# Kernel tuning notes

Measured on AMD Instinct MI355X. Metric: run time of the kernel, lower is better.

Reference implementation:

```python
import jax, jax.numpy as jnp
import numpy as np

N, E, D, H, G = 50000, 800000, 128, 128, 64
EPS = 1e-5


def setup_inputs() -> dict:
    key = jax.random.key(0)
    ks = jax.random.split(key, 16)
    x = jax.random.normal(ks[0], (N, D), dtype=jnp.float32)
    edge_index = jax.random.randint(ks[1], (2, E), 0, N, dtype=jnp.int64)
    batch = jnp.sort(jax.random.randint(ks[2], (N,), 0, G, dtype=jnp.int64))
    dims = [D, H, H, H]
    params = {}
    for i in range(3):
        params[f"W{i}"] = jax.random.normal(ks[3 + i], (dims[i], dims[i + 1]), dtype=jnp.float32) * (1.0 / np.sqrt(dims[i]).astype(np.float32))
        params[f"b{i}"] = jnp.zeros((dims[i + 1],), jnp.float32)
        params[f"g{i}"] = jnp.ones((dims[i + 1],), jnp.float32)   # BN gamma
        params[f"be{i}"] = jnp.zeros((dims[i + 1],), jnp.float32)  # BN beta
    params["Wout"] = jax.random.normal(ks[10], (H, 1), dtype=jnp.float32) * (1.0 / np.sqrt(H).astype(np.float32))
    params["bout"] = jnp.zeros((1,), jnp.float32)
    return {"x": x, "edge_index": edge_index, "batch": batch, **params}


def _gcn_forward(x, edge_index, batch, Ws, bs, gs, bes, Wout, bout):
    n = x.shape[0]
    loop = jnp.arange(n)
    # GCNConv default: add self-loops, symmetric degree normalization
    src = jnp.concatenate([edge_index[0], loop])
    dst = jnp.concatenate([edge_index[1], loop])
    deg = jax.ops.segment_sum(jnp.ones_like(dst, x.dtype), dst, num_segments=n)
    dinv = jax.lax.rsqrt(jnp.maximum(deg, 1.0))  # deg >= 1 from self-loops
    norm = dinv[src] * dinv[dst]                 # [E+N]
    h = x
    for W, b, g, be in zip(Ws, bs, gs, bes):
        h = h @ W                                               # transform [N,C]
        msg = h[src] * norm[:, None]                            # gather [E+N,C]
        h = jax.ops.segment_sum(msg, dst, num_segments=n) + b   # scatter-add
        # BatchNorm1d (training-mode batch statistics over nodes)
        mu = jnp.mean(h, axis=0)
        var = jnp.var(h, axis=0)
        h = (h - mu) * jax.lax.rsqrt(var + EPS) * g + be
        h = jax.nn.relu(h)
        # dropout: identity (deterministic eval reference)
    counts = jax.ops.segment_sum(jnp.ones((n,), h.dtype), batch, num_segments=G)
    pooled = jax.ops.segment_sum(h, batch, num_segments=G) / jnp.maximum(counts, 1.0)[:, None]
    return jax.nn.sigmoid(pooled @ Wout + bout)  # [G,1]


def reference(x, edge_index, batch, W0, b0, g0, be0, W1, b1, g1, be1, W2, b2, g2, be2, Wout, bout):
    return _gcn_forward(x, edge_index, batch,
                        (W0, W1, W2), (b0, b1, b2), (g0, g1, g2), (be0, be1, be2),
                        Wout, bout)
```

## Files before the change

### kernel.cpp

```cpp
#include <hip/hip_runtime.h>

#define EPSBN 1e-5f
#define AGG_BLOCKS 2048

using bf16x8 = __attribute__((ext_vector_type(8))) short;
using f32x4  = __attribute__((ext_vector_type(4))) float;

__device__ __forceinline__ unsigned short f2bf(float f) {
    unsigned u = __builtin_bit_cast(unsigned, f);
    unsigned r = (u + 0x7FFFu + ((u >> 16) & 1u)) >> 16;
    return (unsigned short)r;
}
__device__ __forceinline__ float bf2f(unsigned short s) {
    unsigned u = ((unsigned)s) << 16;
    return __builtin_bit_cast(float, u);
}


__global__ __launch_bounds__(256) void k_bhist(const int* __restrict__ dst, int E,
                                               int* __restrict__ deg, int* __restrict__ bcnt, int shift) {
    __shared__ int lh[512];
    for (int i = threadIdx.x; i < 512; i += 256) lh[i] = 0;
    __syncthreads();
    for (int i = blockIdx.x * blockDim.x + threadIdx.x; i < E; i += gridDim.x * blockDim.x) {
        int d = dst[i];
        atomicAdd(&deg[d], 1);
        atomicAdd(&lh[d >> shift], 1);
    }
    __syncthreads();
    for (int i = threadIdx.x; i < 512; i += 256)
        if (lh[i]) atomicAdd(&bcnt[i], lh[i]);
}

__global__ void k_dinv(const int* __restrict__ deg, int N, float* __restrict__ dinv) {
    int i = blockIdx.x * blockDim.x + threadIdx.x;
    if (i < N) dinv[i] = rsqrtf((float)(deg[i] + 1));
}

__global__ void k_scan1(const int* __restrict__ deg, int N, int* __restrict__ rs, int* __restrict__ blk) {
    __shared__ int sh[256];
    int tid = threadIdx.x;
    int i = blockIdx.x * 256 + tid;
    int v = (i < N) ? deg[i] : 0;
    sh[tid] = v; __syncthreads();
    for (int off = 1; off < 256; off <<= 1) {
        int t = (tid >= off) ? sh[tid - off] : 0;
        __syncthreads();
        sh[tid] += t;
        __syncthreads();
    }
    if (i < N) rs[i] = sh[tid] - v;
    if (tid == 255) blk[blockIdx.x] = sh[255];
}

__global__ void k_scan2(const int* __restrict__ blk, int nb, int* __restrict__ blkoff) {
    __shared__ int sh[1024];
    int tid = threadIdx.x;
    int v = (tid < nb) ? blk[tid] : 0;
    sh[tid] = v; __syncthreads();
    for (int off = 1; off < 1024; off <<= 1) {
        int t = (tid >= off) ? sh[tid - off] : 0;
        __syncthreads();
        sh[tid] += t;
        __syncthreads();
    }
    if (tid < nb) blkoff[tid] = sh[tid] - v;
}

__global__ void k_scan3(int* __restrict__ rs, int N, const int* __restrict__ blkoff) {
    int i = blockIdx.x * blockDim.x + threadIdx.x;
    if (i < N) rs[i] += blkoff[i >> 8];
}


__global__ __launch_bounds__(256) void k_bscatter(const int* __restrict__ src, const int* __restrict__ dst, int E,
                                                  const int* __restrict__ boff, int* __restrict__ gcur,
                                                  uint2* __restrict__ ebuf, int shift) {
    __shared__ int lh[512], lb[512];
    int tid = threadIdx.x;
    int base = blockIdx.x * 2048;
    for (int i = tid; i < 512; i += 256) lh[i] = 0;
    __syncthreads();
    int ms[8], md[8];
    #pragma unroll
    for (int j = 0; j < 8; ++j) {
        int idx = base + j * 256 + tid;
        if (idx < E) {
            ms[j] = src[idx]; md[j] = dst[idx];
            atomicAdd(&lh[md[j] >> shift], 1);
        } else md[j] = -1;
    }
    __syncthreads();
    for (int b = tid; b < 512; b += 256) {
        int c = lh[b];
        lb[b] = c ? atomicAdd(&gcur[b], c) : 0;
    }
    __syncthreads();
    for (int i = tid; i < 512; i += 256) lh[i] = 0;
    __syncthreads();
    #pragma unroll
    for (int j = 0; j < 8; ++j) {
        if (md[j] >= 0) {
            int b = md[j] >> shift;
            int r = atomicAdd(&lh[b], 1);
            ebuf[boff[b] + lb[b] + r] = make_uint2((unsigned)ms[j], (unsigned)md[j]);
        }
    }
}


__global__ __launch_bounds__(256) void k_fill2(const uint2* __restrict__ ebuf, const int* __restrict__ bcnt,
                                               const int* __restrict__ boff, const int* __restrict__ rs,
                                               const float* __restrict__ dinv,
                                               uint2* __restrict__ colw, int shift) {
    __shared__ int lcur[256];
    int b = blockIdx.x;
    int n0 = b << shift;
    int cnt = bcnt[b], s = boff[b];
    int span = 1 << shift;
    for (int i = threadIdx.x; i < span; i += 256) lcur[i] = 0;
    __syncthreads();
    for (int i = threadIdx.x; i < cnt; i += 256) {
        uint2 e = ebuf[s + i];
        int d = (int)e.y;
        int sv = (int)e.x;
        int pos = rs[d] + atomicAdd(&lcur[d - n0], 1);
        colw[pos] = make_uint2((unsigned)sv, __builtin_bit_cast(unsigned, dinv[sv]));
    }
}


__global__ __launch_bounds__(256) void k_wprep(const float* __restrict__ W0, const float* __restrict__ W1,
                                               const float* __restrict__ W2, unsigned short* __restrict__ Wimg) {
    const float* W = (blockIdx.x == 0) ? W0 : (blockIdx.x == 1) ? W1 : W2;
    unsigned short* out = Wimg + (size_t)blockIdx.x * 16384;
    int tid = threadIdx.x;
    int n = tid & 127, kh = tid >> 7;
    const float* wp = &W[(kh * 64) * 128 + n];
    #pragma unroll
    for (int kb = 0; kb < 8; ++kb) {
        unsigned short t8[8];
        #pragma unroll
        for (int e = 0; e < 8; ++e)
            t8[e] = f2bf(wp[(kb * 8 + e) * 128]);
        int byte = (n * 256 + kh * 128 + kb * 16) ^ ((n & 7) << 4);
        *reinterpret_cast<uint4*>(reinterpret_cast<char*>(out) + byte) =
            *reinterpret_cast<const uint4*>(t8);
    }
}


__global__ __launch_bounds__(256) void k_gemm(const unsigned short* __restrict__ Abf,
                                              const float* __restrict__ Af,
                                              const unsigned short* __restrict__ Wimg,
                                              unsigned short* __restrict__ C, int N,
                                              const float* __restrict__ scale,
                                              const float* __restrict__ shift, int mode) {
    __shared__ unsigned short Asw[128 * 128];
    __shared__ unsigned short Wt[128 * 128];
    int tid = threadIdx.x;
    int r0 = blockIdx.x * 128;

    {
        const uint4* wi = reinterpret_cast<const uint4*>(Wimg);
        uint4* wl = reinterpret_cast<uint4*>(Wt);
        #pragma unroll
        for (int j = 0; j < 8; ++j)
            wl[tid + j * 256] = wi[tid + j * 256];
    }
    if (mode == 0) {
        const float* ap = &Af[(size_t)r0 * 128];
        #pragma unroll
        for (int j = 0; j < 8; ++j) {
            int u = tid + j * 256;
            int row = u >> 4, cg = u & 15;
            unsigned short t8[8] = {0,0,0,0,0,0,0,0};
            if (r0 + row < N) {
                float4 a0 = *reinterpret_cast<const float4*>(ap + row * 128 + cg * 8);
                float4 a1 = *reinterpret_cast<const float4*>(ap + row * 128 + cg * 8 + 4);
                t8[0]=f2bf(a0.x); t8[1]=f2bf(a0.y); t8[2]=f2bf(a0.z); t8[3]=f2bf(a0.w);
                t8[4]=f2bf(a1.x); t8[5]=f2bf(a1.y); t8[6]=f2bf(a1.z); t8[7]=f2bf(a1.w);
            }
            int byte = (row * 256 + cg * 16) ^ ((row & 7) << 4);
            *reinterpret_cast<uint4*>(reinterpret_cast<char*>(Asw) + byte) =
                *reinterpret_cast<const uint4*>(t8);
        }
    } else {
        const unsigned short* ap = &Abf[(size_t)r0 * 128];
        #pragma unroll
        for (int j = 0; j < 8; ++j) {
            int u = tid + j * 256;
            int row = u >> 4, cg = u & 15;
            unsigned short t8[8] = {0,0,0,0,0,0,0,0};
            if (r0 + row < N) {
                ushort4 v0 = *reinterpret_cast<const ushort4*>(ap + (size_t)row * 128 + cg * 8);
                ushort4 v1 = *reinterpret_cast<const ushort4*>(ap + (size_t)row * 128 + cg * 8 + 4);
                float4 sc0 = *reinterpret_cast<const float4*>(&scale[cg * 8]);
                float4 sc1 = *reinterpret_cast<const float4*>(&scale[cg * 8 + 4]);
                float4 sf0 = *reinterpret_cast<const float4*>(&shift[cg * 8]);
                float4 sf1 = *reinterpret_cast<const float4*>(&shift[cg * 8 + 4]);
                t8[0] = f2bf(fmaxf(bf2f(v0.x) * sc0.x + sf0.x, 0.f));
                t8[1] = f2bf(fmaxf(bf2f(v0.y) * sc0.y + sf0.y, 0.f));
                t8[2] = f2bf(fmaxf(bf2f(v0.z) * sc0.z + sf0.z, 0.f));
                t8[3] = f2bf(fmaxf(bf2f(v0.w) * sc0.w + sf0.w, 0.f));
                t8[4] = f2bf(fmaxf(bf2f(v1.x) * sc1.x + sf1.x, 0.f));
                t8[5] = f2bf(fmaxf(bf2f(v1.y) * sc1.y + sf1.y, 0.f));
                t8[6] = f2bf(fmaxf(bf2f(v1.z) * sc1.z + sf1.z, 0.f));
                t8[7] = f2bf(fmaxf(bf2f(v1.w) * sc1.w + sf1.w, 0.f));
            }
            int byte = (row * 256 + cg * 16) ^ ((row & 7) << 4);
            *reinterpret_cast<uint4*>(reinterpret_cast<char*>(Asw) + byte) =
                *reinterpret_cast<const uint4*>(t8);
        }
    }
    __syncthreads();

    int wv = tid >> 6, lane = tid & 63;
    int lr = lane & 15, lk = lane >> 4;
    f32x4 acc[2][8] = {};
    #pragma unroll
    for (int kk = 0; kk < 4; ++kk) {
        bf16x8 af[2], bf[8];
        #pragma unroll
        for (int mf = 0; mf < 2; ++mf) {
            int ar = wv * 32 + mf * 16 + lr;
            int byte = (ar * 256 + kk * 64 + lk * 16) ^ ((ar & 7) << 4);
            af[mf] = *reinterpret_cast<const bf16x8*>(reinterpret_cast<const char*>(Asw) + byte);
        }
        #pragma unroll
        for (int nf = 0; nf < 8; ++nf) {
            int bn = nf * 16 + lr;
            int byte = (bn * 256 + kk * 64 + lk * 16) ^ ((bn & 7) << 4);
            bf[nf] = *reinterpret_cast<const bf16x8*>(reinterpret_cast<const char*>(Wt) + byte);
        }
        #pragma unroll
        for (int mf = 0; mf < 2; ++mf)
            #pragma unroll
            for (int nf = 0; nf < 8; ++nf)
                acc[mf][nf] = __builtin_amdgcn_mfma_f32_16x16x32_bf16(af[mf], bf[nf], acc[mf][nf], 0, 0, 0);
    }
    __syncthreads();
    #pragma unroll
    for (int mf = 0; mf < 2; ++mf)
        #pragma unroll
        for (int nf = 0; nf < 8; ++nf)
            #pragma unroll
            for (int r = 0; r < 4; ++r) {
                int row = wv * 32 + mf * 16 + lk * 4 + r;
                int colc = nf * 16 + lr;
                Asw[row * 128 + colc] = f2bf(acc[mf][nf][r]);
            }
    __syncthreads();
    #pragma unroll
    for (int j = 0; j < 8; ++j) {
        int u = tid + j * 256;
        int row = u >> 4, cg = u & 15;
        if (r0 + row < N)
            *reinterpret_cast<uint4*>(&C[((size_t)(r0 + row)) * 128 + cg * 8]) =
                *reinterpret_cast<const uint4*>(&Asw[row * 128 + cg * 8]);
    }
}


__global__ __launch_bounds__(256) void k_agg(const unsigned short* __restrict__ t, const uint2* __restrict__ colw,
                                             const int* __restrict__ rs, const int* __restrict__ deg,
                                             const float* __restrict__ dinv, const float* __restrict__ bias,
                                             unsigned short* __restrict__ out, int N,
                                             float* __restrict__ p1, float* __restrict__ p2) {
    __shared__ uint2 ec[4][64];
    __shared__ float sh[4][64][4];
    int wv = threadIdx.x >> 6, lane = threadIdx.x & 63;
    const ushort2* tp = reinterpret_cast<const ushort2*>(t);
    float b0 = bias[2 * lane], b1 = bias[2 * lane + 1];
    float s1x = 0.f, s1y = 0.f, s2x = 0.f, s2y = 0.f;
    for (int w = blockIdx.x * 4 + wv; w < N; w += gridDim.x * 4) {
        int start = rs[w], cnt = deg[w];
        float di = dinv[w];
        float ax = 0.f, ay = 0.f;
        for (int base = 0; base < cnt; base += 64) {
            int m = min(cnt - base, 64);
            if (lane < m) ec[wv][lane] = colw[start + base + lane];
            asm volatile("s_waitcnt lgkmcnt(0)" ::: "memory");
            int e = 0;
            for (; e + 4 <= m; e += 4) {
                uint2 e0 = ec[wv][e], e1 = ec[wv][e + 1], e2 = ec[wv][e + 2], e3 = ec[wv][e + 3];
                ushort2 v0 = tp[(size_t)e0.x * 64 + lane];
                ushort2 v1 = tp[(size_t)e1.x * 64 + lane];
                ushort2 v2 = tp[(size_t)e2.x * 64 + lane];
                ushort2 v3 = tp[(size_t)e3.x * 64 + lane];
                float w0 = __builtin_bit_cast(float, e0.y), w1 = __builtin_bit_cast(float, e1.y);
                float w2 = __builtin_bit_cast(float, e2.y), w3 = __builtin_bit_cast(float, e3.y);
                ax += w0 * bf2f(v0.x) + w1 * bf2f(v1.x) + w2 * bf2f(v2.x) + w3 * bf2f(v3.x);
                ay += w0 * bf2f(v0.y) + w1 * bf2f(v1.y) + w2 * bf2f(v2.y) + w3 * bf2f(v3.y);
            }
            for (; e < m; ++e) {
                uint2 ee = ec[wv][e];
                ushort2 v = tp[(size_t)ee.x * 64 + lane];
                float ww = __builtin_bit_cast(float, ee.y);
                ax += ww * bf2f(v.x);
                ay += ww * bf2f(v.y);
            }
        }
        ushort2 self = tp[(size_t)w * 64 + lane];
        ushort2 o;
        o.x = f2bf(di * ax + di * di * bf2f(self.x) + b0);
        o.y = f2bf(di * ay + di * di * bf2f(self.y) + b1);
        reinterpret_cast<ushort2*>(out)[(size_t)w * 64 + lane] = o;
        float rx = bf2f(o.x), ry = bf2f(o.y);
        s1x += rx; s1y += ry; s2x += rx * rx; s2y += ry * ry;
    }
    sh[wv][lane][0] = s1x; sh[wv][lane][1] = s1y; sh[wv][lane][2] = s2x; sh[wv][lane][3] = s2y;
    __syncthreads();
    int tid = threadIdx.x;
    if (tid < 64) {
        float a0 = 0.f, a1 = 0.f, a2 = 0.f, a3 = 0.f;
        #pragma unroll
        for (int r = 0; r < 4; ++r) {
            a0 += sh[r][tid][0]; a1 += sh[r][tid][1];
            a2 += sh[r][tid][2]; a3 += sh[r][tid][3];
        }
        p1[blockIdx.x * 128 + 2 * tid]     = a0;
        p1[blockIdx.x * 128 + 2 * tid + 1] = a1;
        p2[blockIdx.x * 128 + 2 * tid]     = a2;
        p2[blockIdx.x * 128 + 2 * tid + 1] = a3;
    }
}


__global__ __launch_bounds__(128) void k_statsmid(const float* __restrict__ p1, const float* __restrict__ p2,
                                                  int rows, float* __restrict__ pm1, float* __restrict__ pm2) {
    int c = threadIdx.x, b = blockIdx.x;
    int r0 = b * rows;
    float s1 = 0.f, s2 = 0.f;
    #pragma unroll 4
    for (int r = 0; r < rows; ++r) {
        s1 += p1[(size_t)(r0 + r) * 128 + c];
        s2 += p2[(size_t)(r0 + r) * 128 + c];
    }
    pm1[b * 128 + c] = s1;
    pm2[b * 128 + c] = s2;
}

__global__ __launch_bounds__(1024) void k_stats2(const float* __restrict__ p1, const float* __restrict__ p2,
                                                 int nb, int N,
                                                 const float* __restrict__ g, const float* __restrict__ be,
                                                 float* __restrict__ scale, float* __restrict__ shift) {
    __shared__ double sh1[1024], sh2[1024];
    int tid = threadIdx.x;
    int c = tid & 127, seg = tid >> 7;
    double s1 = 0.0, s2 = 0.0;
    int b = seg;
    for (; b + 32 <= nb; b += 32) {
        double a0 = p1[(b      ) * 128 + c], q0 = p2[(b      ) * 128 + c];
        double a1 = p1[(b +  8) * 128 + c], q1 = p2[(b +  8) * 128 + c];
        double a2 = p1[(b + 16) * 128 + c], q2 = p2[(b + 16) * 128 + c];
        double a3 = p1[(b + 24) * 128 + c], q3 = p2[(b + 24) * 128 + c];
        s1 += (a0 + a1) + (a2 + a3);
        s2 += (q0 + q1) + (q2 + q3);
    }
    for (; b < nb; b += 8) { s1 += p1[b * 128 + c]; s2 += p2[b * 128 + c]; }
    sh1[tid] = s1; sh2[tid] = s2;
    __syncthreads();
    #pragma unroll
    for (int s = 4; s >= 1; s >>= 1) {
        if (seg < s) {
            sh1[tid] += sh1[tid + s * 128];
            sh2[tid] += sh2[tid + s * 128];
        }
        __syncthreads();
    }
    if (tid < 128) {
        double mu = sh1[c] / N;
        double var = sh2[c] / N - mu * mu;
        double inv = 1.0 / sqrt(var + (double)EPSBN);
        scale[c] = (float)((double)g[c] * inv);
        shift[c] = (float)((double)be[c] - mu * (double)g[c] * inv);
    }
// ... 57 lines not shown
__global__ void k_final(const float* __restrict__ pool, const int* __restrict__ cnt,
                        const float* __restrict__ bout, int G, float* __restrict__ out) {
    int g = blockIdx.x * blockDim.x + threadIdx.x;
    if (g < G) {
        float c = fmaxf((float)cnt[g], 1.f);
        float p = pool[g] / c + bout[0];
        out[g] = 1.f / (1.f + expf(-p));
    }
}


extern "C" void kernel_launch(void* const* d_in, const int* in_sizes, int n_in,
                              void* d_out, int out_size, void* d_ws, size_t ws_size,
                              hipStream_t stream) {
    const float* x    = (const float*)d_in[0];
    const int*   ei   = (const int*)d_in[1];
    const int*   batch= (const int*)d_in[2];
    const float* W0p  = (const float*)d_in[3];
    const float* b0p  = (const float*)d_in[4];
    const float* g0p  = (const float*)d_in[5];
    const float* be0p = (const float*)d_in[6];
    const float* W1p  = (const float*)d_in[7];
    const float* b1p  = (const float*)d_in[8];
    const float* g1p  = (const float*)d_in[9];
    const float* be1p = (const float*)d_in[10];
    const float* W2p  = (const float*)d_in[11];
    const float* b2p  = (const float*)d_in[12];
    const float* g2p  = (const float*)d_in[13];
    const float* be2p = (const float*)d_in[14];
    const float* Woutp= (const float*)d_in[15];
    const float* boutp= (const float*)d_in[16];

    int N = in_sizes[0] / 128;
    int E = in_sizes[1] / 2;
    int G = out_size;
    const int* src = ei;
    const int* dst = ei + E;

    int shiftB = 7;
    while ((((N + (1 << shiftB) - 1) >> shiftB) > 512) && shiftB < 8) ++shiftB;
    int nbuck = (N + (1 << shiftB) - 1) >> shiftB;

    char* p = (char*)d_ws;
    auto alloc = [&](size_t bytes) {
        void* q = (void*)p;
        p += (bytes + 255) & ~(size_t)255;
        return q;
    };
    unsigned short* Bt  = (unsigned short*)alloc((size_t)N * 128 * 2);
    unsigned short* Bh  = (unsigned short*)alloc((size_t)N * 128 * 2);
    uint2*  colw   = (uint2*) alloc((size_t)E * 8);
    uint2*  ebuf   = (uint2*) alloc((size_t)E * 8);
    int*    rsA    = (int*)   alloc((size_t)N * 4);
    int*    deg    = (int*)   alloc((size_t)N * 4);
    float*  dinv   = (float*) alloc((size_t)N * 4);
    int*    blk    = (int*)   alloc(1024 * 4);
    int*    blkoff = (int*)   alloc(1024 * 4);
    int*    bcnt   = (int*)   alloc(512 * 4);
    int*    boff   = (int*)   alloc(512 * 4);
    int*    gcur   = (int*)   alloc(512 * 4);
    unsigned short* Wimg = (unsigned short*)alloc(3 * 16384 * 2);
    float*  p1     = (float*) alloc((size_t)AGG_BLOCKS * 128 * 4);
    float*  p2     = (float*) alloc((size_t)AGG_BLOCKS * 128 * 4);
    float*  pm1    = (float*) alloc(128 * 128 * 4);
    float*  pm2    = (float*) alloc(128 * 128 * 4);
    float*  scale  = (float*) alloc(128 * 4);
    float*  shift  = (float*) alloc(128 * 4);
    float*  pool   = (float*) alloc(64 * 4);
    int*    cnt    = (int*)   alloc(64 * 4);

    hipMemsetAsync(deg, 0, (size_t)N * 4, stream);
    hipMemsetAsync(bcnt, 0, 512 * 4, stream);
    hipMemsetAsync(gcur, 0, 512 * 4, stream);
    hipMemsetAsync(pool, 0, 64 * 4, stream);
    hipMemsetAsync(cnt, 0, 64 * 4, stream);

    int nb = (N + 255) / 256;
    k_wprep   <<<3, 256, 0, stream>>>(W0p, W1p, W2p, Wimg);
    k_bhist   <<<256, 256, 0, stream>>>(dst, E, deg, bcnt, shiftB);
    k_dinv    <<<nb, 256, 0, stream>>>(deg, N, dinv);
    k_scan1   <<<nb, 256, 0, stream>>>(deg, N, rsA, blk);
    k_scan2   <<<1, 1024, 0, stream>>>(blk, nb, blkoff);
    k_scan3   <<<nb, 256, 0, stream>>>(rsA, N, blkoff);
    k_scan2   <<<1, 1024, 0, stream>>>(bcnt, 512, boff);
    k_bscatter<<<(E + 2047) / 2048, 256, 0, stream>>>(src, dst, E, boff, gcur, ebuf, shiftB);
    k_fill2   <<<nbuck, 256, 0, stream>>>(ebuf, bcnt, boff, rsA, dinv, colw, shiftB);

    int gemmBlocks = (N + 127) / 128;
    int midRows = AGG_BLOCKS / 128;

    k_gemm    <<<gemmBlocks, 256, 0, stream>>>(nullptr, x, Wimg, Bt, N, scale, shift, 0);
    k_agg     <<<AGG_BLOCKS, 256, 0, stream>>>(Bt, colw, rsA, deg, dinv, b0p, Bh, N, p1, p2);
    k_statsmid<<<128, 128, 0, stream>>>(p1, p2, midRows, pm1, pm2);
    k_stats2  <<<1, 1024, 0, stream>>>(pm1, pm2, 128, N, g0p, be0p, scale, shift);
    k_gemm    <<<gemmBlocks, 256, 0, stream>>>(Bh, nullptr, Wimg + 16384, Bt, N, scale, shift, 1);
    k_agg     <<<AGG_BLOCKS, 256, 0, stream>>>(Bt, colw, rsA, deg, dinv, b1p, Bh, N, p1, p2);
    k_statsmid<<<128, 128, 0, stream>>>(p1, p2, midRows, pm1, pm2);
    k_stats2  <<<1, 1024, 0, stream>>>(pm1, pm2, 128, N, g1p, be1p, scale, shift);
    k_gemm    <<<gemmBlocks, 256, 0, stream>>>(Bh, nullptr, Wimg + 32768, Bt, N, scale, shift, 1);
    k_agg     <<<AGG_BLOCKS, 256, 0, stream>>>(Bt, colw, rsA, deg, dinv, b2p, Bh, N, p1, p2);
    k_statsmid<<<128, 128, 0, stream>>>(p1, p2, midRows, pm1, pm2);
    k_stats2  <<<1, 1024, 0, stream>>>(pm1, pm2, 128, N, g2p, be2p, scale, shift);
    k_pool <<<256, 256, 0, stream>>>(Bh, batch, scale, shift, Woutp, N, G, pool, cnt);
    k_final<<<1, 64, 0, stream>>>(pool, cnt, boutp, G, (float*)d_out);
}
```

Measured before the change: 290.4 us.

## Vectorize aggregation gathers, shrink GEMM tile, fuse dinv into scan, merge memsets

The aggregation kernel now has each quarter-wave gather a full 128-column row as 16-byte loads, so one wave processes four edges at once. Partial sums are combined with cross-lane shuffles before the output and BatchNorm statistics are written. The GEMM row tile drops from 128 to 64 rows to launch more blocks. The dinv computation moves into the first scan kernel, and the five memsets collapse into one contiguous memset. Together these cut per-edge load instruction count and launch overhead, but the aggregation kernel adds shuffle work and higher register pressure from the 8-wide accumulators.

```diff
diff --git a/kernel.cpp b/kernel.cpp
--- a/kernel.cpp
+++ b/kernel.cpp
@@ -16,6 +16,17 @@
     return __builtin_bit_cast(float, u);
 }
 
+__device__ __forceinline__ void acc8(float* ax, uint4 r, float w) {
+    unsigned rr[4] = {r.x, r.y, r.z, r.w};
+    #pragma unroll
+    for (int j = 0; j < 4; ++j) {
+        float lo = __builtin_bit_cast(float, rr[j] << 16);
+        float hi = __builtin_bit_cast(float, rr[j] & 0xFFFF0000u);
+        ax[2 * j]     += w * lo;
+        ax[2 * j + 1] += w * hi;
+    }
+}
+
 
 __global__ __launch_bounds__(256) void k_bhist(const int* __restrict__ dst, int E,
                                                int* __restrict__ deg, int* __restrict__ bcnt, int shift) {
@@ -32,16 +43,13 @@
         if (lh[i]) atomicAdd(&bcnt[i], lh[i]);
 }
 
-__global__ void k_dinv(const int* __restrict__ deg, int N, float* __restrict__ dinv) {
-    int i = blockIdx.x * blockDim.x + threadIdx.x;
-    if (i < N) dinv[i] = rsqrtf((float)(deg[i] + 1));
-}
-
-__global__ void k_scan1(const int* __restrict__ deg, int N, int* __restrict__ rs, int* __restrict__ blk) {
+__global__ void k_scan1(const int* __restrict__ deg, int N, int* __restrict__ rs, int* __restrict__ blk,
+                        float* __restrict__ dinv) {
     __shared__ int sh[256];
     int tid = threadIdx.x;
     int i = blockIdx.x * 256 + tid;
     int v = (i < N) ? deg[i] : 0;
+    if (i < N) dinv[i] = rsqrtf((float)(v + 1));
     sh[tid] = v; __syncthreads();
     for (int off = 1; off < 256; off <<= 1) {
         int t = (tid >= off) ? sh[tid - off] : 0;
@@ -156,10 +164,10 @@
                                               unsigned short* __restrict__ C, int N,
                                               const float* __restrict__ scale,
                                               const float* __restrict__ shift, int mode) {
-    __shared__ unsigned short Asw[128 * 128];
+    __shared__ unsigned short Asw[64 * 128];
     __shared__ unsigned short Wt[128 * 128];
     int tid = threadIdx.x;
-    int r0 = blockIdx.x * 128;
+    int r0 = blockIdx.x * 64;
 
     {
         const uint4* wi = reinterpret_cast<const uint4*>(Wimg);
@@ -171,7 +179,7 @@
     if (mode == 0) {
         const float* ap = &Af[(size_t)r0 * 128];
         #pragma unroll
-        for (int j = 0; j < 8; ++j) {
+        for (int j = 0; j < 4; ++j) {
             int u = tid + j * 256;
             int row = u >> 4, cg = u & 15;
             unsigned short t8[8] = {0,0,0,0,0,0,0,0};
@@ -188,7 +196,7 @@
     } else {
         const unsigned short* ap = &Abf[(size_t)r0 * 128];
         #pragma unroll
-        for (int j = 0; j < 8; ++j) {
+        for (int j = 0; j < 4; ++j) {
             int u = tid + j * 256;
             int row = u >> 4, cg = u & 15;
             unsigned short t8[8] = {0,0,0,0,0,0,0,0};
@@ -217,16 +225,13 @@
 
     int wv = tid >> 6, lane = tid & 63;
     int lr = lane & 15, lk = lane >> 4;
-    f32x4 acc[2][8] = {};
+    f32x4 acc[8] = {};
     #pragma unroll
     for (int kk = 0; kk < 4; ++kk) {
-        bf16x8 af[2], bf[8];
-        #pragma unroll
-        for (int mf = 0; mf < 2; ++mf) {
-            int ar = wv * 32 + mf * 16 + lr;
-            int byte = (ar * 256 + kk * 64 + lk * 16) ^ ((ar & 7) << 4);
-            af[mf] = *reinterpret_cast<const bf16x8*>(reinterpret_cast<const char*>(Asw) + byte);
-        }
+        int ar = wv * 16 + lr;
+        int abyte = (ar * 256 + kk * 64 + lk * 16) ^ ((ar & 7) << 4);
+        bf16x8 af = *reinterpret_cast<const bf16x8*>(reinterpret_cast<const char*>(Asw) + abyte);
+        bf16x8 bf[8];
         #pragma unroll
         for (int nf = 0; nf < 8; ++nf) {
             int bn = nf * 16 + lr;
@@ -234,25 +239,21 @@
             bf[nf] = *reinterpret_cast<const bf16x8*>(reinterpret_cast<const char*>(Wt) + byte);
         }
         #pragma unroll
-        for (int mf = 0; mf < 2; ++mf)
-            #pragma unroll
-            for (int nf = 0; nf < 8; ++nf)
-                acc[mf][nf] = __builtin_amdgcn_mfma_f32_16x16x32_bf16(af[mf], bf[nf], acc[mf][nf], 0, 0, 0);
-    }
-    __syncthreads();
-    #pragma unroll
-    for (int mf = 0; mf < 2; ++mf)
-        #pragma unroll
         for (int nf = 0; nf < 8; ++nf)
-            #pragma unroll
-            for (int r = 0; r < 4; ++r) {
-                int row = wv * 32 + mf * 16 + lk * 4 + r;
-                int colc = nf * 16 + lr;
-                Asw[row * 128 + colc] = f2bf(acc[mf][nf][r]);
-            }
-    __syncthreads();
-    #pragma unroll
-    for (int j = 0; j < 8; ++j) {
+            acc[nf] = __builtin_amdgcn_mfma_f32_16x16x32_bf16(af, bf[nf], acc[nf], 0, 0, 0);
+    }
+    __syncthreads();
+    #pragma unroll
+    for (int nf = 0; nf < 8; ++nf)
+        #pragma unroll
+        for (int r = 0; r < 4; ++r) {
+            int row = wv * 16 + lk * 4 + r;
+            int colc = nf * 16 + lr;
+            Asw[row * 128 + colc] = f2bf(acc[nf][r]);
+        }
+    __syncthreads();
+    #pragma unroll
+    for (int j = 0; j < 4; ++j) {
         int u = tid + j * 256;
         int row = u >> 4, cg = u & 15;
         if (r0 + row < N)
@@ -268,61 +269,87 @@
                                              unsigned short* __restrict__ out, int N,
                                              float* __restrict__ p1, float* __restrict__ p2) {
     __shared__ uint2 ec[4][64];
-    __shared__ float sh[4][64][4];
+    __shared__ float shs[4][16][8][2];
     int wv = threadIdx.x >> 6, lane = threadIdx.x & 63;
-    const ushort2* tp = reinterpret_cast<const ushort2*>(t);
-    float b0 = bias[2 * lane], b1 = bias[2 * lane + 1];
-    float s1x = 0.f, s1y = 0.f, s2x = 0.f, s2y = 0.f;
+    int q = lane >> 4, l = lane & 15;
+    const uint4* tp8 = reinterpret_cast<const uint4*>(t);
+    float b8[8];
+    {
+        float4 ba = *reinterpret_cast<const float4*>(&bias[l * 8]);
+        float4 bb = *reinterpret_cast<const float4*>(&bias[l * 8 + 4]);
+        b8[0]=ba.x; b8[1]=ba.y; b8[2]=ba.z; b8[3]=ba.w;
+        b8[4]=bb.x; b8[5]=bb.y; b8[6]=bb.z; b8[7]=bb.w;
+    }
+    float s1[8] = {}, s2[8] = {};
     for (int w = blockIdx.x * 4 + wv; w < N; w += gridDim.x * 4) {
         int start = rs[w], cnt = deg[w];
         float di = dinv[w];
-        float ax = 0.f, ay = 0.f;
+        float ax[8] = {};
         for (int base = 0; base < cnt; base += 64) {
             int m = min(cnt - base, 64);
             if (lane < m) ec[wv][lane] = colw[start + base + lane];
             asm volatile("s_waitcnt lgkmcnt(0)" ::: "memory");
-            int e = 0;
-            for (; e + 4 <= m; e += 4) {
-                uint2 e0 = ec[wv][e], e1 = ec[wv][e + 1], e2 = ec[wv][e + 2], e3 = ec[wv][e + 3];
-                ushort2 v0 = tp[(size_t)e0.x * 64 + lane];
-                ushort2 v1 = tp[(size_t)e1.x * 64 + lane];
-                ushort2 v2 = tp[(size_t)e2.x * 64 + lane];
-                ushort2 v3 = tp[(size_t)e3.x * 64 + lane];
-                float w0 = __builtin_bit_cast(float, e0.y), w1 = __builtin_bit_cast(float, e1.y);
-                float w2 = __builtin_bit_cast(float, e2.y), w3 = __builtin_bit_cast(float, e3.y);
-                ax += w0 * bf2f(v0.x) + w1 * bf2f(v1.x) + w2 * bf2f(v2.x) + w3 * bf2f(v3.x);
-                ay += w0 * bf2f(v0.y) + w1 * bf2f(v1.y) + w2 * bf2f(v2.y) + w3 * bf2f(v3.y);
+            int steps = m >> 2, rem = m & 3;
+            int s = 0;
+            for (; s + 2 <= steps; s += 2) {
+                uint2 m0 = ec[wv][(s << 2) + q];
+                uint2 m1 = ec[wv][(s << 2) + 4 + q];
+                uint4 r0 = tp8[(size_t)m0.x * 16 + l];
+                uint4 r1 = tp8[(size_t)m1.x * 16 + l];
+                acc8(ax, r0, __builtin_bit_cast(float, m0.y));
+                acc8(ax, r1, __builtin_bit_cast(float, m1.y));
             }
-            for (; e < m; ++e) {
-                uint2 ee = ec[wv][e];
-                ushort2 v = tp[(size_t)ee.x * 64 + lane];
-                float ww = __builtin_bit_cast(float, ee.y);
-                ax += ww * bf2f(v.x);
-                ay += ww * bf2f(v.y);
+            if (s < steps) {
+                uint2 m0 = ec[wv][(s << 2) + q];
+                uint4 r0 = tp8[(size_t)m0.x * 16 + l];
+                acc8(ax, r0, __builtin_bit_cast(float, m0.y));
             }
-        }
-        ushort2 self = tp[(size_t)w * 64 + lane];
-        ushort2 o;
-        o.x = f2bf(di * ax + di * di * bf2f(self.x) + b0);
-        o.y = f2bf(di * ay + di * di * bf2f(self.y) + b1);
-        reinterpret_cast<ushort2*>(out)[(size_t)w * 64 + lane] = o;
-        float rx = bf2f(o.x), ry = bf2f(o.y);
-        s1x += rx; s1y += ry; s2x += rx * rx; s2y += ry * ry;
-    }
-    sh[wv][lane][0] = s1x; sh[wv][lane][1] = s1y; sh[wv][lane][2] = s2x; sh[wv][lane][3] = s2y;
-    __syncthreads();
-    int tid = threadIdx.x;
-    if (tid < 64) {
-        float a0 = 0.f, a1 = 0.f, a2 = 0.f, a3 = 0.f;
-        #pragma unroll
-        for (int r = 0; r < 4; ++r) {
-            a0 += sh[r][tid][0]; a1 += sh[r][tid][1];
-            a2 += sh[r][tid][2]; a3 += sh[r][tid][3];
-        }
-        p1[blockIdx.x * 128 + 2 * tid]     = a0;
-        p1[blockIdx.x * 128 + 2 * tid + 1] = a1;
-        p2[blockIdx.x * 128 + 2 * tid]     = a2;
-        p2[blockIdx.x * 128 + 2 * tid + 1] = a3;
+            if (q < rem) {
+                uint2 m0 = ec[wv][(steps << 2) + q];
+                uint4 r0 = tp8[(size_t)m0.x * 16 + l];
+                acc8(ax, r0, __builtin_bit_cast(float, m0.y));
+            }
+        }
+        #pragma unroll
+        for (int j = 0; j < 8; ++j) {
+            float v = ax[j];
+            v += __shfl_down(v, 32);
+            v += __shfl_down(v, 16);
+            ax[j] = v;
+        }
+        if (q == 0) {
+            uint4 sr = tp8[(size_t)w * 16 + l];
+            unsigned sw_[4] = {sr.x, sr.y, sr.z, sr.w};
+            unsigned short ov[8];
+            float d2 = di * di;
+            #pragma unroll
+            for (int j = 0; j < 8; ++j) {
+                unsigned uw = sw_[j >> 1];
+                float sv = (j & 1) ? __builtin_bit_cast(float, uw & 0xFFFF0000u)
+                                   : __builtin_bit_cast(float, uw << 16);
+                float r = di * ax[j] + d2 * sv + b8[j];
+                unsigned short us = f2bf(r);
+                ov[j] = us;
+                float rr = bf2f(us);
+                s1[j] += rr; s2[j] += rr * rr;
+            }
+            *reinterpret_cast<uint4*>(&out[(size_t)w * 128 + l * 8]) =
+                *reinterpret_cast<const uint4*>(ov);
+        }
+    }
+    if (q == 0) {
+        #pragma unroll
+        for (int j = 0; j < 8; ++j) { shs[wv][l][j][0] = s1[j]; shs[wv][l][j][1] = s2[j]; }
+    }
+    __syncthreads();
+    int tid = threadIdx.x;
+    if (tid < 128) {
+        int ll = tid >> 3, jj = tid & 7;
+        float a1 = 0.f, a2 = 0.f;
+        #pragma unroll
+        for (int r = 0; r < 4; ++r) { a1 += shs[r][ll][jj][0]; a2 += shs[r][ll][jj][1]; }
+        p1[blockIdx.x * 128 + tid] = a1;
+        p2[blockIdx.x * 128 + tid] = a2;
     }
 }
 
@@ -486,13 +513,10 @@
     uint2*  colw   = (uint2*) alloc((size_t)E * 8);
     uint2*  ebuf   = (uint2*) alloc((size_t)E * 8);
     int*    rsA    = (int*)   alloc((size_t)N * 4);
-    int*    deg    = (int*)   alloc((size_t)N * 4);
     float*  dinv   = (float*) alloc((size_t)N * 4);
     int*    blk    = (int*)   alloc(1024 * 4);
     int*    blkoff = (int*)   alloc(1024 * 4);
-    int*    bcnt   = (int*)   alloc(512 * 4);
     int*    boff   = (int*)   alloc(512 * 4);
-    int*    gcur   = (int*)   alloc(512 * 4);
     unsigned short* Wimg = (unsigned short*)alloc(3 * 16384 * 2);
     float*  p1     = (float*) alloc((size_t)AGG_BLOCKS * 128 * 4);
     float*  p2     = (float*) alloc((size_t)AGG_BLOCKS * 128 * 4);
@@ -500,27 +524,27 @@
     float*  pm2    = (float*) alloc(128 * 128 * 4);
     float*  scale  = (float*) alloc(128 * 4);
     float*  shift  = (float*) alloc(128 * 4);
+    char*   z0     = p;
+    int*    deg    = (int*)   alloc((size_t)N * 4);
+    int*    bcnt   = (int*)   alloc(512 * 4);
+    int*    gcur   = (int*)   alloc(512 * 4);
     float*  pool   = (float*) alloc(64 * 4);
     int*    cnt    = (int*)   alloc(64 * 4);
-
-    hipMemsetAsync(deg, 0, (size_t)N * 4, stream);
-    hipMemsetAsync(bcnt, 0, 512 * 4, stream);
-    hipMemsetAsync(gcur, 0, 512 * 4, stream);
-    hipMemsetAsync(pool, 0, 64 * 4, stream);
-    hipMemsetAsync(cnt, 0, 64 * 4, stream);
+    size_t  zbytes = (size_t)(p - z0);
+
+    hipMemsetAsync(z0, 0, zbytes, stream);
 
     int nb = (N + 255) / 256;
     k_wprep   <<<3, 256, 0, stream>>>(W0p, W1p, W2p, Wimg);
     k_bhist   <<<256, 256, 0, stream>>>(dst, E, deg, bcnt, shiftB);
-    k_dinv    <<<nb, 256, 0, stream>>>(deg, N, dinv);
-    k_scan1   <<<nb, 256, 0, stream>>>(deg, N, rsA, blk);
+    k_scan1   <<<nb, 256, 0, stream>>>(deg, N, rsA, blk, dinv);
     k_scan2   <<<1, 1024, 0, stream>>>(blk, nb, blkoff);
     k_scan3   <<<nb, 256, 0, stream>>>(rsA, N, blkoff);
     k_scan2   <<<1, 1024, 0, stream>>>(bcnt, 512, boff);
     k_bscatter<<<(E + 2047) / 2048, 256, 0, stream>>>(src, dst, E, boff, gcur, ebuf, shiftB);
     k_fill2   <<<nbuck, 256, 0, stream>>>(ebuf, bcnt, boff, rsA, dinv, colw, shiftB);
 
-    int gemmBlocks = (N + 127) / 128;
+    int gemmBlocks = (N + 63) / 64;
     int midRows = AGG_BLOCKS / 128;
 
     k_gemm    <<<gemmBlocks, 256, 0, stream>>>(nullptr, x, Wimg, Bt, N, scale, shift, 0);
```

Result: slower. 315.4 us (+8.6%).

## Fuse dinv into scan, halve GEMM tile, dual-node aggregation, merge memsets

Applied to the files above, without the earlier changes.

Computes dinv inside the first scan kernel, which removes one launch. The GEMM row tile shrinks from 128 to 64 rows per block, giving more blocks and less shared memory per block. The aggregation kernel now processes two destination nodes per wavefront at once to raise memory-level parallelism on the gathers. The zero-initialised buffers are placed next to each other and cleared with one memset instead of five. Interleaving two nodes risks imbalance when the two degrees differ, and the smaller tile reloads W more often.

```diff
diff --git a/kernel.cpp b/kernel.cpp
--- a/kernel.cpp
+++ b/kernel.cpp
@@ -32,16 +32,13 @@
         if (lh[i]) atomicAdd(&bcnt[i], lh[i]);
 }
 
-__global__ void k_dinv(const int* __restrict__ deg, int N, float* __restrict__ dinv) {
-    int i = blockIdx.x * blockDim.x + threadIdx.x;
-    if (i < N) dinv[i] = rsqrtf((float)(deg[i] + 1));
-}
-
-__global__ void k_scan1(const int* __restrict__ deg, int N, int* __restrict__ rs, int* __restrict__ blk) {
+__global__ void k_scan1(const int* __restrict__ deg, int N, int* __restrict__ rs, int* __restrict__ blk,
+                        float* __restrict__ dinv) {
     __shared__ int sh[256];
     int tid = threadIdx.x;
     int i = blockIdx.x * 256 + tid;
     int v = (i < N) ? deg[i] : 0;
+    if (i < N) dinv[i] = rsqrtf((float)(v + 1));
     sh[tid] = v; __syncthreads();
     for (int off = 1; off < 256; off <<= 1) {
         int t = (tid >= off) ? sh[tid - off] : 0;
@@ -156,10 +153,10 @@
                                               unsigned short* __restrict__ C, int N,
                                               const float* __restrict__ scale,
                                               const float* __restrict__ shift, int mode) {
-    __shared__ unsigned short Asw[128 * 128];
+    __shared__ unsigned short Asw[64 * 128];
     __shared__ unsigned short Wt[128 * 128];
     int tid = threadIdx.x;
-    int r0 = blockIdx.x * 128;
+    int r0 = blockIdx.x * 64;
 
     {
         const uint4* wi = reinterpret_cast<const uint4*>(Wimg);
@@ -171,7 +168,7 @@
     if (mode == 0) {
         const float* ap = &Af[(size_t)r0 * 128];
         #pragma unroll
-        for (int j = 0; j < 8; ++j) {
+        for (int j = 0; j < 4; ++j) {
             int u = tid + j * 256;
             int row = u >> 4, cg = u & 15;
             unsigned short t8[8] = {0,0,0,0,0,0,0,0};
@@ -188,7 +185,7 @@
     } else {
         const unsigned short* ap = &Abf[(size_t)r0 * 128];
         #pragma unroll
-        for (int j = 0; j < 8; ++j) {
+        for (int j = 0; j < 4; ++j) {
             int u = tid + j * 256;
             int row = u >> 4, cg = u & 15;
             unsigned short t8[8] = {0,0,0,0,0,0,0,0};
@@ -217,16 +214,13 @@
 
     int wv = tid >> 6, lane = tid & 63;
     int lr = lane & 15, lk = lane >> 4;
-    f32x4 acc[2][8] = {};
+    f32x4 acc[8] = {};
     #pragma unroll
     for (int kk = 0; kk < 4; ++kk) {
-        bf16x8 af[2], bf[8];
-        #pragma unroll
-        for (int mf = 0; mf < 2; ++mf) {
-            int ar = wv * 32 + mf * 16 + lr;
-            int byte = (ar * 256 + kk * 64 + lk * 16) ^ ((ar & 7) << 4);
-            af[mf] = *reinterpret_cast<const bf16x8*>(reinterpret_cast<const char*>(Asw) + byte);
-        }
+        int ar = wv * 16 + lr;
+        int abyte = (ar * 256 + kk * 64 + lk * 16) ^ ((ar & 7) << 4);
+        bf16x8 af = *reinterpret_cast<const bf16x8*>(reinterpret_cast<const char*>(Asw) + abyte);
+        bf16x8 bf[8];
         #pragma unroll
         for (int nf = 0; nf < 8; ++nf) {
             int bn = nf * 16 + lr;
@@ -234,25 +228,21 @@
             bf[nf] = *reinterpret_cast<const bf16x8*>(reinterpret_cast<const char*>(Wt) + byte);
         }
         #pragma unroll
-        for (int mf = 0; mf < 2; ++mf)
-            #pragma unroll
-            for (int nf = 0; nf < 8; ++nf)
-                acc[mf][nf] = __builtin_amdgcn_mfma_f32_16x16x32_bf16(af[mf], bf[nf], acc[mf][nf], 0, 0, 0);
-    }
-    __syncthreads();
-    #pragma unroll
-    for (int mf = 0; mf < 2; ++mf)
-        #pragma unroll
         for (int nf = 0; nf < 8; ++nf)
-            #pragma unroll
-            for (int r = 0; r < 4; ++r) {
-                int row = wv * 32 + mf * 16 + lk * 4 + r;
-                int colc = nf * 16 + lr;
-                Asw[row * 128 + colc] = f2bf(acc[mf][nf][r]);
-            }
-    __syncthreads();
-    #pragma unroll
-    for (int j = 0; j < 8; ++j) {
+            acc[nf] = __builtin_amdgcn_mfma_f32_16x16x32_bf16(af, bf[nf], acc[nf], 0, 0, 0);
+    }
+    __syncthreads();
+    #pragma unroll
+    for (int nf = 0; nf < 8; ++nf)
+        #pragma unroll
+        for (int r = 0; r < 4; ++r) {
+            int row = wv * 16 + lk * 4 + r;
+            int colc = nf * 16 + lr;
+            Asw[row * 128 + colc] = f2bf(acc[nf][r]);
+        }
+    __syncthreads();
+    #pragma unroll
+    for (int j = 0; j < 4; ++j) {
         int u = tid + j * 256;
         int row = u >> 4, cg = u & 15;
         if (r0 + row < N)
@@ -267,47 +257,82 @@
                                              const float* __restrict__ dinv, const float* __restrict__ bias,
                                              unsigned short* __restrict__ out, int N,
                                              float* __restrict__ p1, float* __restrict__ p2) {
-    __shared__ uint2 ec[4][64];
+    __shared__ uint2 ec[4][2][64];
     __shared__ float sh[4][64][4];
     int wv = threadIdx.x >> 6, lane = threadIdx.x & 63;
     const ushort2* tp = reinterpret_cast<const ushort2*>(t);
     float b0 = bias[2 * lane], b1 = bias[2 * lane + 1];
     float s1x = 0.f, s1y = 0.f, s2x = 0.f, s2y = 0.f;
-    for (int w = blockIdx.x * 4 + wv; w < N; w += gridDim.x * 4) {
-        int start = rs[w], cnt = deg[w];
-        float di = dinv[w];
-        float ax = 0.f, ay = 0.f;
-        for (int base = 0; base < cnt; base += 64) {
-            int m = min(cnt - base, 64);
-            if (lane < m) ec[wv][lane] = colw[start + base + lane];
+    int stride = gridDim.x * 4;
+    for (int w = blockIdx.x * 4 + wv; w < N; w += 2 * stride) {
+        int wB = w + stride;
+        bool hasB = wB < N;
+        int stA = rs[w], cntA = deg[w];
+        int stB = hasB ? rs[wB] : 0, cntB = hasB ? deg[wB] : 0;
+        float diA = dinv[w], diB = hasB ? dinv[wB] : 0.f;
+        float axA = 0.f, ayA = 0.f, axB = 0.f, ayB = 0.f;
+        int maxc = max(cntA, cntB);
+        for (int base = 0; base < maxc; base += 64) {
+            int mA = min(cntA - base, 64);
+            int mB = min(cntB - base, 64);
+            if (lane < mA) ec[wv][0][lane] = colw[stA + base + lane];
+            if (lane < mB) ec[wv][1][lane] = colw[stB + base + lane];
             asm volatile("s_waitcnt lgkmcnt(0)" ::: "memory");
+            int both = min(mA, mB);
             int e = 0;
-            for (; e + 4 <= m; e += 4) {
-                uint2 e0 = ec[wv][e], e1 = ec[wv][e + 1], e2 = ec[wv][e + 2], e3 = ec[wv][e + 3];
-                ushort2 v0 = tp[(size_t)e0.x * 64 + lane];
-                ushort2 v1 = tp[(size_t)e1.x * 64 + lane];
-                ushort2 v2 = tp[(size_t)e2.x * 64 + lane];
-                ushort2 v3 = tp[(size_t)e3.x * 64 + lane];
-                float w0 = __builtin_bit_cast(float, e0.y), w1 = __builtin_bit_cast(float, e1.y);
-                float w2 = __builtin_bit_cast(float, e2.y), w3 = __builtin_bit_cast(float, e3.y);
-                ax += w0 * bf2f(v0.x) + w1 * bf2f(v1.x) + w2 * bf2f(v2.x) + w3 * bf2f(v3.x);
-                ay += w0 * bf2f(v0.y) + w1 * bf2f(v1.y) + w2 * bf2f(v2.y) + w3 * bf2f(v3.y);
+            for (; e + 2 <= both; e += 2) {
+                uint2 a0 = ec[wv][0][e], a1 = ec[wv][0][e + 1];
+                uint2 c0 = ec[wv][1][e], c1 = ec[wv][1][e + 1];
+                ushort2 va0 = tp[(size_t)a0.x * 64 + lane];
+                ushort2 vb0 = tp[(size_t)c0.x * 64 + lane];
+                ushort2 va1 = tp[(size_t)a1.x * 64 + lane];
+                ushort2 vb1 = tp[(size_t)c1.x * 64 + lane];
+                float wa0 = __builtin_bit_cast(float, a0.y), wa1 = __builtin_bit_cast(float, a1.y);
+                float wb0 = __builtin_bit_cast(float, c0.y), wb1 = __builtin_bit_cast(float, c1.y);
+                axA += wa0 * bf2f(va0.x) + wa1 * bf2f(va1.x);
+                ayA += wa0 * bf2f(va0.y) + wa1 * bf2f(va1.y);
+                axB += wb0 * bf2f(vb0.x) + wb1 * bf2f(vb1.x);
+                ayB += wb0 * bf2f(vb0.y) + wb1 * bf2f(vb1.y);
             }
-            for (; e < m; ++e) {
-                uint2 ee = ec[wv][e];
-                ushort2 v = tp[(size_t)ee.x * 64 + lane];
-                float ww = __builtin_bit_cast(float, ee.y);
-                ax += ww * bf2f(v.x);
-                ay += ww * bf2f(v.y);
+            for (; e < both; ++e) {
+                uint2 a0 = ec[wv][0][e], c0 = ec[wv][1][e];
+                ushort2 va = tp[(size_t)a0.x * 64 + lane];
+                ushort2 vb = tp[(size_t)c0.x * 64 + lane];
+                float wa = __builtin_bit_cast(float, a0.y), wb = __builtin_bit_cast(float, c0.y);
+                axA += wa * bf2f(va.x); ayA += wa * bf2f(va.y);
+                axB += wb * bf2f(vb.x); ayB += wb * bf2f(vb.y);
             }
-        }
-        ushort2 self = tp[(size_t)w * 64 + lane];
-        ushort2 o;
-        o.x = f2bf(di * ax + di * di * bf2f(self.x) + b0);
-        o.y = f2bf(di * ay + di * di * bf2f(self.y) + b1);
-        reinterpret_cast<ushort2*>(out)[(size_t)w * 64 + lane] = o;
-        float rx = bf2f(o.x), ry = bf2f(o.y);
-        s1x += rx; s1y += ry; s2x += rx * rx; s2y += ry * ry;
+            for (; e < mA; ++e) {
+                uint2 a0 = ec[wv][0][e];
+                ushort2 va = tp[(size_t)a0.x * 64 + lane];
+                float wa = __builtin_bit_cast(float, a0.y);
+                axA += wa * bf2f(va.x); ayA += wa * bf2f(va.y);
+            }
+            for (; e < mB; ++e) {
+                uint2 c0 = ec[wv][1][e];
+                ushort2 vb = tp[(size_t)c0.x * 64 + lane];
+                float wb = __builtin_bit_cast(float, c0.y);
+                axB += wb * bf2f(vb.x); ayB += wb * bf2f(vb.y);
+            }
+        }
+        {
+            ushort2 selfA = tp[(size_t)w * 64 + lane];
+            ushort2 oA;
+            oA.x = f2bf(diA * axA + diA * diA * bf2f(selfA.x) + b0);
+            oA.y = f2bf(diA * ayA + diA * diA * bf2f(selfA.y) + b1);
+            reinterpret_cast<ushort2*>(out)[(size_t)w * 64 + lane] = oA;
+            float rx = bf2f(oA.x), ry = bf2f(oA.y);
+            s1x += rx; s1y += ry; s2x += rx * rx; s2y += ry * ry;
+        }
+        if (hasB) {
+            ushort2 selfB = tp[(size_t)wB * 64 + lane];
+            ushort2 oB;
+            oB.x = f2bf(diB * axB + diB * diB * bf2f(selfB.x) + b0);
+            oB.y = f2bf(diB * ayB + diB * diB * bf2f(selfB.y) + b1);
+            reinterpret_cast<ushort2*>(out)[(size_t)wB * 64 + lane] = oB;
+            float rx = bf2f(oB.x), ry = bf2f(oB.y);
+            s1x += rx; s1y += ry; s2x += rx * rx; s2y += ry * ry;
+        }
     }
     sh[wv][lane][0] = s1x; sh[wv][lane][1] = s1y; sh[wv][lane][2] = s2x; sh[wv][lane][3] = s2y;
     __syncthreads();
@@ -486,13 +511,10 @@
     uint2*  colw   = (uint2*) alloc((size_t)E * 8);
     uint2*  ebuf   = (uint2*) alloc((size_t)E * 8);
     int*    rsA    = (int*)   alloc((size_t)N * 4);
-    int*    deg    = (int*)   alloc((size_t)N * 4);
     float*  dinv   = (float*) alloc((size_t)N * 4);
     int*    blk    = (int*)   alloc(1024 * 4);
     int*    blkoff = (int*)   alloc(1024 * 4);
-    int*    bcnt   = (int*)   alloc(512 * 4);
     int*    boff   = (int*)   alloc(512 * 4);
-    int*    gcur   = (int*)   alloc(512 * 4);
     unsigned short* Wimg = (unsigned short*)alloc(3 * 16384 * 2);
     float*  p1     = (float*) alloc((size_t)AGG_BLOCKS * 128 * 4);
     float*  p2     = (float*) alloc((size_t)AGG_BLOCKS * 128 * 4);
@@ -500,27 +522,27 @@
     float*  pm2    = (float*) alloc(128 * 128 * 4);
     float*  scale  = (float*) alloc(128 * 4);
     float*  shift  = (float*) alloc(128 * 4);
+    char*   z0     = p;
+    int*    deg    = (int*)   alloc((size_t)N * 4);
+    int*    bcnt   = (int*)   alloc(512 * 4);
+    int*    gcur   = (int*)   alloc(512 * 4);
     float*  pool   = (float*) alloc(64 * 4);
     int*    cnt    = (int*)   alloc(64 * 4);
-
-    hipMemsetAsync(deg, 0, (size_t)N * 4, stream);
-    hipMemsetAsync(bcnt, 0, 512 * 4, stream);
-    hipMemsetAsync(gcur, 0, 512 * 4, stream);
-    hipMemsetAsync(pool, 0, 64 * 4, stream);
-    hipMemsetAsync(cnt, 0, 64 * 4, stream);
+    size_t  zbytes = (size_t)(p - z0);
+
+    hipMemsetAsync(z0, 0, zbytes, stream);
 
     int nb = (N + 255) / 256;
     k_wprep   <<<3, 256, 0, stream>>>(W0p, W1p, W2p, Wimg);
     k_bhist   <<<256, 256, 0, stream>>>(dst, E, deg, bcnt, shiftB);
-    k_dinv    <<<nb, 256, 0, stream>>>(deg, N, dinv);
-    k_scan1   <<<nb, 256, 0, stream>>>(deg, N, rsA, blk);
+    k_scan1   <<<nb, 256, 0, stream>>>(deg, N, rsA, blk, dinv);
     k_scan2   <<<1, 1024, 0, stream>>>(blk, nb, blkoff);
     k_scan3   <<<nb, 256, 0, stream>>>(rsA, N, blkoff);
     k_scan2   <<<1, 1024, 0, stream>>>(bcnt, 512, boff);
     k_bscatter<<<(E + 2047) / 2048, 256, 0, stream>>>(src, dst, E, boff, gcur, ebuf, shiftB);
     k_fill2   <<<nbuck, 256, 0, stream>>>(ebuf, bcnt, boff, rsA, dinv, colw, shiftB);
 
-    int gemmBlocks = (N + 127) / 128;
+    int gemmBlocks = (N + 63) / 64;
     int midRows = AGG_BLOCKS / 128;
 
     k_gemm    <<<gemmBlocks, 256, 0, stream>>>(nullptr, x, Wimg, Bt, N, scale, shift, 0);
```

Measured after the change: 297.8 us. +2.5%, slower.

## Fuse setup kernels, merge memsets, halve GEMM row tile, widen pool grid

Applied to the files above, without the earlier changes.

The dinv computation moves into the first scan kernel, and the two small scans become one two-block launch. The five memsets are replaced by a single contiguous memset, which trims launch and setup overhead. The GEMM tile drops from 128 to 64 rows per block, giving more blocks across the CUs at the cost of reloading the weight tile more often. The pooling grid is widened from 256 to 1024 blocks, which adds more atomic contention on the pool buffers.

```diff
diff --git a/kernel.cpp b/kernel.cpp
--- a/kernel.cpp
+++ b/kernel.cpp
@@ -32,16 +32,13 @@
         if (lh[i]) atomicAdd(&bcnt[i], lh[i]);
 }
 
-__global__ void k_dinv(const int* __restrict__ deg, int N, float* __restrict__ dinv) {
-    int i = blockIdx.x * blockDim.x + threadIdx.x;
-    if (i < N) dinv[i] = rsqrtf((float)(deg[i] + 1));
-}
-
-__global__ void k_scan1(const int* __restrict__ deg, int N, int* __restrict__ rs, int* __restrict__ blk) {
+__global__ void k_scan1(const int* __restrict__ deg, int N, int* __restrict__ rs, int* __restrict__ blk,
+                        float* __restrict__ dinv) {
     __shared__ int sh[256];
     int tid = threadIdx.x;
     int i = blockIdx.x * 256 + tid;
     int v = (i < N) ? deg[i] : 0;
+    if (i < N) dinv[i] = rsqrtf((float)(v + 1));
     sh[tid] = v; __syncthreads();
     for (int off = 1; off < 256; off <<= 1) {
         int t = (tid >= off) ? sh[tid - off] : 0;
@@ -53,10 +50,14 @@
     if (tid == 255) blk[blockIdx.x] = sh[255];
 }
 
-__global__ void k_scan2(const int* __restrict__ blk, int nb, int* __restrict__ blkoff) {
+__global__ __launch_bounds__(1024) void k_scan2x(const int* __restrict__ blk, int nb, int* __restrict__ blkoff,
+                                                 const int* __restrict__ bcnt, int nb2, int* __restrict__ boff) {
     __shared__ int sh[1024];
-    int tid = threadIdx.x;
-    int v = (tid < nb) ? blk[tid] : 0;
+    const int* in = blockIdx.x ? bcnt : blk;
+    int n = blockIdx.x ? nb2 : nb;
+    int* outp = blockIdx.x ? boff : blkoff;
+    int tid = threadIdx.x;
+    int v = (tid < n) ? in[tid] : 0;
     sh[tid] = v; __syncthreads();
     for (int off = 1; off < 1024; off <<= 1) {
         int t = (tid >= off) ? sh[tid - off] : 0;
@@ -64,7 +65,7 @@
         sh[tid] += t;
         __syncthreads();
     }
-    if (tid < nb) blkoff[tid] = sh[tid] - v;
+    if (tid < n) outp[tid] = sh[tid] - v;
 }
 
 __global__ void k_scan3(int* __restrict__ rs, int N, const int* __restrict__ blkoff) {
@@ -156,10 +157,10 @@
                                               unsigned short* __restrict__ C, int N,
                                               const float* __restrict__ scale,
                                               const float* __restrict__ shift, int mode) {
-    __shared__ unsigned short Asw[128 * 128];
+    __shared__ unsigned short Asw[64 * 128];
     __shared__ unsigned short Wt[128 * 128];
     int tid = threadIdx.x;
-    int r0 = blockIdx.x * 128;
+    int r0 = blockIdx.x * 64;
 
     {
         const uint4* wi = reinterpret_cast<const uint4*>(Wimg);
@@ -171,7 +172,7 @@
     if (mode == 0) {
         const float* ap = &Af[(size_t)r0 * 128];
         #pragma unroll
-        for (int j = 0; j < 8; ++j) {
+        for (int j = 0; j < 4; ++j) {
             int u = tid + j * 256;
             int row = u >> 4, cg = u & 15;
             unsigned short t8[8] = {0,0,0,0,0,0,0,0};
@@ -188,7 +189,7 @@
     } else {
         const unsigned short* ap = &Abf[(size_t)r0 * 128];
         #pragma unroll
-        for (int j = 0; j < 8; ++j) {
+        for (int j = 0; j < 4; ++j) {
             int u = tid + j * 256;
             int row = u >> 4, cg = u & 15;
             unsigned short t8[8] = {0,0,0,0,0,0,0,0};
@@ -217,16 +218,13 @@
 
     int wv = tid >> 6, lane = tid & 63;
     int lr = lane & 15, lk = lane >> 4;
-    f32x4 acc[2][8] = {};
+    f32x4 acc[8] = {};
     #pragma unroll
     for (int kk = 0; kk < 4; ++kk) {
-        bf16x8 af[2], bf[8];
-        #pragma unroll
-        for (int mf = 0; mf < 2; ++mf) {
-            int ar = wv * 32 + mf * 16 + lr;
-            int byte = (ar * 256 + kk * 64 + lk * 16) ^ ((ar & 7) << 4);
-            af[mf] = *reinterpret_cast<const bf16x8*>(reinterpret_cast<const char*>(Asw) + byte);
-        }
+        int ar = wv * 16 + lr;
+        int abyte = (ar * 256 + kk * 64 + lk * 16) ^ ((ar & 7) << 4);
+        bf16x8 af = *reinterpret_cast<const bf16x8*>(reinterpret_cast<const char*>(Asw) + abyte);
+        bf16x8 bf[8];
         #pragma unroll
         for (int nf = 0; nf < 8; ++nf) {
             int bn = nf * 16 + lr;
@@ -234,25 +232,21 @@
             bf[nf] = *reinterpret_cast<const bf16x8*>(reinterpret_cast<const char*>(Wt) + byte);
         }
         #pragma unroll
-        for (int mf = 0; mf < 2; ++mf)
-            #pragma unroll
-            for (int nf = 0; nf < 8; ++nf)
-                acc[mf][nf] = __builtin_amdgcn_mfma_f32_16x16x32_bf16(af[mf], bf[nf], acc[mf][nf], 0, 0, 0);
-    }
-    __syncthreads();
-    #pragma unroll
-    for (int mf = 0; mf < 2; ++mf)
-        #pragma unroll
         for (int nf = 0; nf < 8; ++nf)
-            #pragma unroll
-            for (int r = 0; r < 4; ++r) {
-                int row = wv * 32 + mf * 16 + lk * 4 + r;
-                int colc = nf * 16 + lr;
-                Asw[row * 128 + colc] = f2bf(acc[mf][nf][r]);
-            }
-    __syncthreads();
-    #pragma unroll
-    for (int j = 0; j < 8; ++j) {
+            acc[nf] = __builtin_amdgcn_mfma_f32_16x16x32_bf16(af, bf[nf], acc[nf], 0, 0, 0);
+    }
+    __syncthreads();
+    #pragma unroll
+    for (int nf = 0; nf < 8; ++nf)
+        #pragma unroll
+        for (int r = 0; r < 4; ++r) {
+            int row = wv * 16 + lk * 4 + r;
+            int colc = nf * 16 + lr;
+            Asw[row * 128 + colc] = f2bf(acc[nf][r]);
+        }
+    __syncthreads();
+    #pragma unroll
+    for (int j = 0; j < 4; ++j) {
         int u = tid + j * 256;
         int row = u >> 4, cg = u & 15;
         if (r0 + row < N)
@@ -486,13 +480,10 @@
     uint2*  colw   = (uint2*) alloc((size_t)E * 8);
     uint2*  ebuf   = (uint2*) alloc((size_t)E * 8);
     int*    rsA    = (int*)   alloc((size_t)N * 4);
-    int*    deg    = (int*)   alloc((size_t)N * 4);
     float*  dinv   = (float*) alloc((size_t)N * 4);
     int*    blk    = (int*)   alloc(1024 * 4);
     int*    blkoff = (int*)   alloc(1024 * 4);
-    int*    bcnt   = (int*)   alloc(512 * 4);
     int*    boff   = (int*)   alloc(512 * 4);
-    int*    gcur   = (int*)   alloc(512 * 4);
     unsigned short* Wimg = (unsigned short*)alloc(3 * 16384 * 2);
     float*  p1     = (float*) alloc((size_t)AGG_BLOCKS * 128 * 4);
     float*  p2     = (float*) alloc((size_t)AGG_BLOCKS * 128 * 4);
@@ -500,27 +491,26 @@
     float*  pm2    = (float*) alloc(128 * 128 * 4);
     float*  scale  = (float*) alloc(128 * 4);
     float*  shift  = (float*) alloc(128 * 4);
+    char*   z0     = p;
+    int*    deg    = (int*)   alloc((size_t)N * 4);
+    int*    bcnt   = (int*)   alloc(512 * 4);
+    int*    gcur   = (int*)   alloc(512 * 4);
     float*  pool   = (float*) alloc(64 * 4);
     int*    cnt    = (int*)   alloc(64 * 4);
-
-    hipMemsetAsync(deg, 0, (size_t)N * 4, stream);
-    hipMemsetAsync(bcnt, 0, 512 * 4, stream);
-    hipMemsetAsync(gcur, 0, 512 * 4, stream);
-    hipMemsetAsync(pool, 0, 64 * 4, stream);
-    hipMemsetAsync(cnt, 0, 64 * 4, stream);
+    size_t  zbytes = (size_t)(p - z0);
+
+    hipMemsetAsync(z0, 0, zbytes, stream);
 
     int nb = (N + 255) / 256;
     k_wprep   <<<3, 256, 0, stream>>>(W0p, W1p, W2p, Wimg);
     k_bhist   <<<256, 256, 0, stream>>>(dst, E, deg, bcnt, shiftB);
-    k_dinv    <<<nb, 256, 0, stream>>>(deg, N, dinv);
-    k_scan1   <<<nb, 256, 0, stream>>>(deg, N, rsA, blk);
-    k_scan2   <<<1, 1024, 0, stream>>>(blk, nb, blkoff);
+    k_scan1   <<<nb, 256, 0, stream>>>(deg, N, rsA, blk, dinv);
+    k_scan2x  <<<2, 1024, 0, stream>>>(blk, nb, blkoff, bcnt, 512, boff);
     k_scan3   <<<nb, 256, 0, stream>>>(rsA, N, blkoff);
-    k_scan2   <<<1, 1024, 0, stream>>>(bcnt, 512, boff);
     k_bscatter<<<(E + 2047) / 2048, 256, 0, stream>>>(src, dst, E, boff, gcur, ebuf, shiftB);
     k_fill2   <<<nbuck, 256, 0, stream>>>(ebuf, bcnt, boff, rsA, dinv, colw, shiftB);
 
-    int gemmBlocks = (N + 127) / 128;
+    int gemmBlocks = (N + 63) / 64;
     int midRows = AGG_BLOCKS / 128;
 
     k_gemm    <<<gemmBlocks, 256, 0, stream>>>(nullptr, x, Wimg, Bt, N, scale, shift, 0);
@@ -535,6 +525,6 @@
     k_agg     <<<AGG_BLOCKS, 256, 0, stream>>>(Bt, colw, rsA, deg, dinv, b2p, Bh, N, p1, p2);
     k_statsmid<<<128, 128, 0, stream>>>(p1, p2, midRows, pm1, pm2);
     k_stats2  <<<1, 1024, 0, stream>>>(pm1, pm2, 128, N, g2p, be2p, scale, shift);
-    k_pool <<<256, 256, 0, stream>>>(Bh, batch, scale, shift, Woutp, N, G, pool, cnt);
+    k_pool <<<1024, 256, 0, stream>>>(Bh, batch, scale, shift, Woutp, N, G, pool, cnt);
     k_final<<<1, 64, 0, stream>>>(pool, cnt, boutp, G, (float*)d_out);
 }
```

Measured after the change: 281.7 us. 1.03x faster.
